# Performance work log

Measured on AMD Instinct MI355X. Metric: run time of the kernel, lower is better.

The kernel has to match this reference:

```python
import jax, jax.numpy as jnp
import numpy as np

B = 262144
INPUT_SIZE = 128
HIDDEN_SIZE = 128
EPS = 1e-08


def rms_norm(x, eps=EPS):
    # NB: despite the name, the original subtracts the mean (LayerNorm without affine)
    mean = jnp.mean(x, axis=-1, keepdims=True)
    var = jnp.var(x, axis=-1, keepdims=True)  # biased, matches unbiased=False
    return (x - mean) / jnp.sqrt(var + eps)


def activation_quant(x):
    s = 127.0 / jnp.max(jnp.abs(x), axis=-1, keepdims=True)
    return jnp.clip(jnp.round(s * x), -128.0, 127.0) / s


def matmul_free_linear(x, w_t):
    # w_t is ternary {-1,0,1}, shape [in, out]; original uses two masked matmuls
    pos = (w_t == 1.0).astype(x.dtype)
    neg = (w_t == -1.0).astype(x.dtype)
    return x @ pos - x @ neg


def setup_inputs() -> dict:
    key = jax.random.key(0)
    k1, k2, k3, k4, k5 = jax.random.split(key, 5)
    return {
        "x_t": jax.random.normal(k1, (B, INPUT_SIZE), dtype=jnp.float32),
        "h_t_minus_1": jax.random.normal(k2, (B, HIDDEN_SIZE), dtype=jnp.float32),
        "W_f": jax.random.normal(k3, (HIDDEN_SIZE, INPUT_SIZE), dtype=jnp.float32) * 0.01,
        "W_c": jax.random.normal(k4, (HIDDEN_SIZE, INPUT_SIZE), dtype=jnp.float32) * 0.01,
        "W_g": jax.random.normal(k5, (HIDDEN_SIZE, INPUT_SIZE), dtype=jnp.float32) * 0.01,
        "b_f": jnp.zeros((HIDDEN_SIZE,), dtype=jnp.float32),
        "b_c": jnp.zeros((HIDDEN_SIZE,), dtype=jnp.float32),
        "b_g": jnp.zeros((HIDDEN_SIZE,), dtype=jnp.float32),
    }


def reference(x_t, h_t_minus_1, W_f, W_c, W_g, b_f, b_c, b_g):
    x = activation_quant(rms_norm(x_t, EPS))
    Wf_t = jnp.sign(W_f).T  # [in, hidden]
    Wc_t = jnp.sign(W_c).T
    Wg_t = jnp.sign(W_g).T
    f_t = jax.nn.sigmoid(matmul_free_linear(x, Wf_t) + b_f)
    c_t = jax.nn.silu(matmul_free_linear(x, Wc_t) + b_c)
    g_t = jax.nn.sigmoid(matmul_free_linear(x, Wg_t) + b_g)
    h_t = f_t * h_t_minus_1 + (1.0 - f_t) * c_t
    o_t = g_t * h_t
    return (o_t, h_t)
```

## Files before the change

### kernel.cpp

```cpp
#include <hip/hip_runtime.h>
#include <math.h>

#define WPB 4
#define RG  8

__device__ __forceinline__ int dot4(int a, int b, int c) {
#if defined(__has_builtin)
#if __has_builtin(__builtin_amdgcn_sdot4)
    return __builtin_amdgcn_sdot4(a, b, c, false);
#define DOT4_DONE 1
#endif
#endif
#ifndef DOT4_DONE
    int r = c;
    r += ((a << 24) >> 24) * ((b << 24) >> 24);
    r += ((a << 16) >> 24) * ((b << 16) >> 24);
    r += ((a <<  8) >> 24) * ((b <<  8) >> 24);
    r += ( a        >> 24) * ( b        >> 24);
    return r;
#endif
}

__device__ __forceinline__ float sigmoidf_(float v) {
    return 1.0f / (1.0f + __expf(-v));
}

__global__ __launch_bounds__(256, 3)
void mlgru_kernel(const float* __restrict__ x,
                  const float* __restrict__ hprev,
                  const float* __restrict__ Wf,
                  const float* __restrict__ Wc,
                  const float* __restrict__ Wg,
                  const float* __restrict__ bf,
                  const float* __restrict__ bc,
                  const float* __restrict__ bg,
                  float* __restrict__ out,
                  int nrows)
{
    __shared__ int   wlds[3 * 32 * 128];
    __shared__ short qlds[WPB][RG][64];

    const int tid  = threadIdx.x;
    const int lane = tid & 63;
    const int widx = tid >> 6;

    for (int idx = tid; idx < 3 * 4096; idx += 256) {
        const int g   = idx >> 12;
        const int rem = idx & 4095;
        const int j   = rem >> 5;
        const int w   = rem & 31;
        const float* Wp = (g == 0) ? Wf : ((g == 1) ? Wc : Wg);
        const float4 v = *(const float4*)(Wp + j * 128 + w * 4);
        const int b0 = (v.x > 0.f) - (v.x < 0.f);
        const int b1 = (v.y > 0.f) - (v.y < 0.f);
        const int b2 = (v.z > 0.f) - (v.z < 0.f);
        const int b3 = (v.w > 0.f) - (v.w < 0.f);
        wlds[g * 4096 + w * 128 + j] =
            (b0 & 0xFF) | ((b1 & 0xFF) << 8) | ((b2 & 0xFF) << 16) | ((b3 & 0xFF) << 24);
    }

    const float2 vbf = *(const float2*)(bf + 2 * lane);
    const float2 vbc = *(const float2*)(bc + 2 * lane);
    const float2 vbg = *(const float2*)(bg + 2 * lane);
    __syncthreads();

    const int gw   = blockIdx.x * WPB + widx;
    const int nw   = gridDim.x * WPB;
    const int ngrp = nrows / RG;
    const long long hoff = (long long)nrows * 128;

    for (int grp = gw; grp < ngrp; grp += nw) {
        const int row0 = grp * RG;

        float invs[RG];
        float2 xv[RG];
        #pragma unroll
        for (int r = 0; r < RG; ++r)
            xv[r] = *(const float2*)(x + (long long)(row0 + r) * 128 + 2 * lane);

        #pragma unroll
        for (int r = 0; r < RG; ++r) {
            float s  = xv[r].x + xv[r].y;
            float ss = xv[r].x * xv[r].x + xv[r].y * xv[r].y;
            #pragma unroll
            for (int off = 32; off >= 1; off >>= 1) {
                s  += __shfl_xor(s, off);
                ss += __shfl_xor(ss, off);
            }
            const float mean = s * (1.0f / 128.0f);
            const float var  = ss * (1.0f / 128.0f) - mean * mean;
            const float rstd = rsqrtf(var + 1e-8f);
            const float y0 = (xv[r].x - mean) * rstd;
            const float y1 = (xv[r].y - mean) * rstd;
            float a = fmaxf(fabsf(y0), fabsf(y1));
            #pragma unroll
            for (int off = 32; off >= 1; off >>= 1)
                a = fmaxf(a, __shfl_xor(a, off));
            const float sq = 127.0f / a;
            invs[r] = a * (1.0f / 127.0f);
            int q0 = (int)rintf(y0 * sq);
            int q1 = (int)rintf(y1 * sq);
            q0 = max(-128, min(127, q0));
            q1 = max(-128, min(127, q1));
            qlds[widx][r][lane] = (short)((q0 & 0xFF) | ((q1 & 0xFF) << 8));
        }
        __asm__ __volatile__("s_waitcnt lgkmcnt(0)" ::: "memory");

        int acc[3][2][RG];
        #pragma unroll
        for (int g = 0; g < 3; ++g)
            #pragma unroll
            for (int h = 0; h < 2; ++h)
                #pragma unroll
                for (int r = 0; r < RG; ++r)
                    acc[g][h][r] = 0;

        const int* qrow = (const int*)(&qlds[widx][0][0]);

        #pragma unroll 2
        for (int w4 = 0; w4 < 8; ++w4) {
            int qa[RG][4];
            #pragma unroll
            for (int r = 0; r < RG; ++r) {
                const int4 t = *(const int4*)(qrow + r * 32 + w4 * 4);
                qa[r][0] = t.x; qa[r][1] = t.y; qa[r][2] = t.z; qa[r][3] = t.w;
            }
            #pragma unroll
            for (int wi = 0; wi < 4; ++wi) {
                const int w = w4 * 4 + wi;
                #pragma unroll
                for (int g = 0; g < 3; ++g) {
                    const int2 wv = *(const int2*)(&wlds[g * 4096 + w * 128 + 2 * lane]);
                    #pragma unroll
                    for (int r = 0; r < RG; ++r) {
                        acc[g][0][r] = dot4(qa[r][wi], wv.x, acc[g][0][r]);
                        acc[g][1][r] = dot4(qa[r][wi], wv.y, acc[g][1][r]);
                    }
                }
            }
        }

        #pragma unroll
        for (int r = 0; r < RG; ++r) {
            const long long rbase = (long long)(row0 + r) * 128 + 2 * lane;
            const float2 hp = *(const float2*)(hprev + rbase);
            const float inv = invs[r];

            const float f0 = sigmoidf_((float)acc[0][0][r] * inv + vbf.x);
            const float f1 = sigmoidf_((float)acc[0][1][r] * inv + vbf.y);
            const float cx0 = (float)acc[1][0][r] * inv + vbc.x;
            const float cx1 = (float)acc[1][1][r] * inv + vbc.y;
            const float c0 = cx0 * sigmoidf_(cx0);
            const float c1 = cx1 * sigmoidf_(cx1);
            const float g0 = sigmoidf_((float)acc[2][0][r] * inv + vbg.x);
            const float g1 = sigmoidf_((float)acc[2][1][r] * inv + vbg.y);

            const float h0 = f0 * hp.x + (1.0f - f0) * c0;
            const float h1 = f1 * hp.y + (1.0f - f1) * c1;
            const float o0 = g0 * h0;
            const float o1 = g1 * h1;

            *(float2*)(out + rbase)        = make_float2(o0, o1);
            *(float2*)(out + hoff + rbase) = make_float2(h0, h1);
        }
    }
}

extern "C" void kernel_launch(void* const* d_in, const int* in_sizes, int n_in,
                              void* d_out, int out_size, void* d_ws, size_t ws_size,
                              hipStream_t stream) {
    const float* x  = (const float*)d_in[0];
    const float* h  = (const float*)d_in[1];
    const float* Wf = (const float*)d_in[2];
    const float* Wc = (const float*)d_in[3];
    const float* Wg = (const float*)d_in[4];
    const float* bf = (const float*)d_in[5];
    const float* bc = (const float*)d_in[6];
    const float* bg = (const float*)d_in[7];
    float* out = (float*)d_out;
    const int nrows = in_sizes[0] / 128;

    hipLaunchKernelGGL(mlgru_kernel, dim3(768), dim3(256), 0, stream,
                       x, h, Wf, Wc, Wg, bf, bc, bg, out, nrows);
}
```

Before: 543.3 us.

## Replace sdot4 int8 GEMM with MFMA i32_16x16x64_i8 matrix cores

```diff
diff --git a/kernel.cpp b/kernel.cpp
--- a/kernel.cpp
+++ b/kernel.cpp
@@ -1,25 +1,8 @@
 #include <hip/hip_runtime.h>
 #include <math.h>
 
-#define WPB 4
-#define RG  8
-
-__device__ __forceinline__ int dot4(int a, int b, int c) {
-#if defined(__has_builtin)
-#if __has_builtin(__builtin_amdgcn_sdot4)
-    return __builtin_amdgcn_sdot4(a, b, c, false);
-#define DOT4_DONE 1
-#endif
-#endif
-#ifndef DOT4_DONE
-    int r = c;
-    r += ((a << 24) >> 24) * ((b << 24) >> 24);
-    r += ((a << 16) >> 24) * ((b << 16) >> 24);
-    r += ((a <<  8) >> 24) * ((b <<  8) >> 24);
-    r += ( a        >> 24) * ( b        >> 24);
-    return r;
-#endif
-}
+typedef __attribute__((ext_vector_type(4))) int   i32x4;
+typedef __attribute__((ext_vector_type(4))) float f32x4;
 
 __device__ __forceinline__ float sigmoidf_(float v) {
     return 1.0f / (1.0f + __expf(-v));
@@ -37,131 +20,145 @@
                   float* __restrict__ out,
                   int nrows)
 {
-    __shared__ int   wlds[3 * 32 * 128];
-    __shared__ short qlds[WPB][RG][64];
+    __shared__ i32x4 wlds[3 * 8 * 2 * 64];
 
     const int tid  = threadIdx.x;
     const int lane = tid & 63;
     const int widx = tid >> 6;
+    const int lm   = lane & 15;
+    const int kg   = lane >> 4;
 
-    for (int idx = tid; idx < 3 * 4096; idx += 256) {
-        const int g   = idx >> 12;
-        const int rem = idx & 4095;
-        const int j   = rem >> 5;
-        const int w   = rem & 31;
+    for (int idx = tid; idx < 3 * 8 * 2 * 64; idx += 256) {
+        const int l  = idx & 63;
+        const int s  = (idx >> 6) & 1;
+        const int t  = (idx >> 7) & 7;
+        const int g  = idx >> 10;
         const float* Wp = (g == 0) ? Wf : ((g == 1) ? Wc : Wg);
-        const float4 v = *(const float4*)(Wp + j * 128 + w * 4);
-        const int b0 = (v.x > 0.f) - (v.x < 0.f);
-        const int b1 = (v.y > 0.f) - (v.y < 0.f);
-        const int b2 = (v.z > 0.f) - (v.z < 0.f);
-        const int b3 = (v.w > 0.f) - (v.w < 0.f);
-        wlds[g * 4096 + w * 128 + j] =
-            (b0 & 0xFF) | ((b1 & 0xFF) << 8) | ((b2 & 0xFF) << 16) | ((b3 & 0xFF) << 24);
+        const int n  = t * 16 + (l & 15);
+        const int kb = s * 64 + (l >> 4) * 16;
+        i32x4 fr;
+        #pragma unroll
+        for (int d = 0; d < 4; ++d) {
+            const float4 v = *(const float4*)(Wp + n * 128 + kb + d * 4);
+            const int b0 = (v.x > 0.f) - (v.x < 0.f);
+            const int b1 = (v.y > 0.f) - (v.y < 0.f);
+            const int b2 = (v.z > 0.f) - (v.z < 0.f);
+            const int b3 = (v.w > 0.f) - (v.w < 0.f);
+            fr[d] = (b0 & 0xFF) | ((b1 & 0xFF) << 8) | ((b2 & 0xFF) << 16) | ((b3 & 0xFF) << 24);
+        }
+        wlds[idx] = fr;
     }
 
-    const float2 vbf = *(const float2*)(bf + 2 * lane);
-    const float2 vbc = *(const float2*)(bc + 2 * lane);
-    const float2 vbg = *(const float2*)(bg + 2 * lane);
+    float vbf[8], vbc[8], vbg[8];
+    #pragma unroll
+    for (int t = 0; t < 8; ++t) {
+        vbf[t] = bf[t * 16 + lm];
+        vbc[t] = bc[t * 16 + lm];
+        vbg[t] = bg[t * 16 + lm];
+    }
     __syncthreads();
 
-    const int gw   = blockIdx.x * WPB + widx;
-    const int nw   = gridDim.x * WPB;
-    const int ngrp = nrows / RG;
+    const int gw   = blockIdx.x * 4 + widx;
+    const int nw   = gridDim.x * 4;
+    const int ngrp = nrows >> 5;
     const long long hoff = (long long)nrows * 128;
 
     for (int grp = gw; grp < ngrp; grp += nw) {
-        const int row0 = grp * RG;
+        const int row0 = grp << 5;
 
-        float invs[RG];
-        float2 xv[RG];
-        #pragma unroll
-        for (int r = 0; r < RG; ++r)
-            xv[r] = *(const float2*)(x + (long long)(row0 + r) * 128 + 2 * lane);
+        i32x4 afrag[2][2];
+        float invm[2];
 
         #pragma unroll
-        for (int r = 0; r < RG; ++r) {
-            float s  = xv[r].x + xv[r].y;
-            float ss = xv[r].x * xv[r].x + xv[r].y * xv[r].y;
+        for (int mt = 0; mt < 2; ++mt) {
+            const float* xr = x + (long long)(row0 + mt * 16 + lm) * 128 + kg * 16;
+            f32x4 vv[8];
             #pragma unroll
-            for (int off = 32; off >= 1; off >>= 1) {
-                s  += __shfl_xor(s, off);
-                ss += __shfl_xor(ss, off);
+            for (int j = 0; j < 4; ++j) {
+                vv[j]     = *(const f32x4*)(xr + j * 4);
+                vv[j + 4] = *(const f32x4*)(xr + 64 + j * 4);
             }
+            float s = 0.f, ss = 0.f;
+            #pragma unroll
+            for (int j = 0; j < 8; ++j)
+                #pragma unroll
+                for (int e = 0; e < 4; ++e) { const float t = vv[j][e]; s += t; ss = fmaf(t, t, ss); }
+            s  += __shfl_xor(s, 16);   ss += __shfl_xor(ss, 16);
+            s  += __shfl_xor(s, 32);   ss += __shfl_xor(ss, 32);
             const float mean = s * (1.0f / 128.0f);
             const float var  = ss * (1.0f / 128.0f) - mean * mean;
             const float rstd = rsqrtf(var + 1e-8f);
-            const float y0 = (xv[r].x - mean) * rstd;
-            const float y1 = (xv[r].y - mean) * rstd;
-            float a = fmaxf(fabsf(y0), fabsf(y1));
+            float am = 0.f;
             #pragma unroll
-            for (int off = 32; off >= 1; off >>= 1)
-                a = fmaxf(a, __shfl_xor(a, off));
-            const float sq = 127.0f / a;
-            invs[r] = a * (1.0f / 127.0f);
-            int q0 = (int)rintf(y0 * sq);
-            int q1 = (int)rintf(y1 * sq);
-            q0 = max(-128, min(127, q0));
-            q1 = max(-128, min(127, q1));
-            qlds[widx][r][lane] = (short)((q0 & 0xFF) | ((q1 & 0xFF) << 8));
-        }
-        __asm__ __volatile__("s_waitcnt lgkmcnt(0)" ::: "memory");
-
-        int acc[3][2][RG];
-        #pragma unroll
-        for (int g = 0; g < 3; ++g)
+            for (int j = 0; j < 8; ++j)
+                #pragma unroll
+                for (int e = 0; e < 4; ++e) {
+                    const float t = vv[j][e] - mean;
+                    vv[j][e] = t;
+                    am = fmaxf(am, fabsf(t));
+                }
+            am = fmaxf(am, __shfl_xor(am, 16));
+            am = fmaxf(am, __shfl_xor(am, 32));
+            const float sq = 127.0f / am;
+            invm[mt] = am * rstd * (1.0f / 127.0f);
             #pragma unroll
-            for (int h = 0; h < 2; ++h)
+            for (int s2 = 0; s2 < 2; ++s2) {
+                i32x4 fr;
                 #pragma unroll
-                for (int r = 0; r < RG; ++r)
-                    acc[g][h][r] = 0;
-
-        const int* qrow = (const int*)(&qlds[widx][0][0]);
-
-        #pragma unroll 2
-        for (int w4 = 0; w4 < 8; ++w4) {
-            int qa[RG][4];
-            #pragma unroll
-            for (int r = 0; r < RG; ++r) {
-                const int4 t = *(const int4*)(qrow + r * 32 + w4 * 4);
-                qa[r][0] = t.x; qa[r][1] = t.y; qa[r][2] = t.z; qa[r][3] = t.w;
-            }
-            #pragma unroll
-            for (int wi = 0; wi < 4; ++wi) {
-                const int w = w4 * 4 + wi;
-                #pragma unroll
-                for (int g = 0; g < 3; ++g) {
-                    const int2 wv = *(const int2*)(&wlds[g * 4096 + w * 128 + 2 * lane]);
-                    #pragma unroll
-                    for (int r = 0; r < RG; ++r) {
-                        acc[g][0][r] = dot4(qa[r][wi], wv.x, acc[g][0][r]);
-                        acc[g][1][r] = dot4(qa[r][wi], wv.y, acc[g][1][r]);
-                    }
+                for (int d = 0; d < 4; ++d) {
+                    const int j = s2 * 4 + d;
+                    const int q0 = max(-128, min(127, (int)rintf(vv[j][0] * sq)));
+                    const int q1 = max(-128, min(127, (int)rintf(vv[j][1] * sq)));
+                    const int q2 = max(-128, min(127, (int)rintf(vv[j][2] * sq)));
+                    const int q3 = max(-128, min(127, (int)rintf(vv[j][3] * sq)));
+                    fr[d] = (q0 & 0xFF) | ((q1 & 0xFF) << 8) | ((q2 & 0xFF) << 16) | ((q3 & 0xFF) << 24);
                 }
+                afrag[mt][s2] = fr;
             }
         }
 
+        float invb[2][4];
         #pragma unroll
-        for (int r = 0; r < RG; ++r) {
-            const long long rbase = (long long)(row0 + r) * 128 + 2 * lane;
-            const float2 hp = *(const float2*)(hprev + rbase);
-            const float inv = invs[r];
+        for (int mt = 0; mt < 2; ++mt)
+            #pragma unroll
+            for (int r = 0; r < 4; ++r)
+                invb[mt][r] = __shfl(invm[mt], kg * 4 + r);
 
-            const float f0 = sigmoidf_((float)acc[0][0][r] * inv + vbf.x);
-            const float f1 = sigmoidf_((float)acc[0][1][r] * inv + vbf.y);
-            const float cx0 = (float)acc[1][0][r] * inv + vbc.x;
-            const float cx1 = (float)acc[1][1][r] * inv + vbc.y;
-            const float c0 = cx0 * sigmoidf_(cx0);
-            const float c1 = cx1 * sigmoidf_(cx1);
-            const float g0 = sigmoidf_((float)acc[2][0][r] * inv + vbg.x);
-            const float g1 = sigmoidf_((float)acc[2][1][r] * inv + vbg.y);
+        for (int t = 0; t < 8; ++t) {
+            i32x4 acc[3][2];
+            #pragma unroll
+            for (int g = 0; g < 3; ++g) {
+                acc[g][0] = (i32x4){0, 0, 0, 0};
+                acc[g][1] = (i32x4){0, 0, 0, 0};
+            }
+            #pragma unroll
+            for (int s2 = 0; s2 < 2; ++s2)
+                #pragma unroll
+                for (int g = 0; g < 3; ++g) {
+                    const i32x4 bfr = wlds[((g * 8 + t) * 2 + s2) * 64 + lane];
+                    acc[g][0] = __builtin_amdgcn_mfma_i32_16x16x64_i8(afrag[0][s2], bfr, acc[g][0], 0, 0, 0);
+                    acc[g][1] = __builtin_amdgcn_mfma_i32_16x16x64_i8(afrag[1][s2], bfr, acc[g][1], 0, 0, 0);
+                }
 
-            const float h0 = f0 * hp.x + (1.0f - f0) * c0;
-            const float h1 = f1 * hp.y + (1.0f - f1) * c1;
-            const float o0 = g0 * h0;
-            const float o1 = g1 * h1;
-
-            *(float2*)(out + rbase)        = make_float2(o0, o1);
-            *(float2*)(out + hoff + rbase) = make_float2(h0, h1);
+            #pragma unroll
+            for (int mt = 0; mt < 2; ++mt)
+                #pragma unroll
+                for (int r = 0; r < 4; ++r) {
+                    const int m = kg * 4 + r;
+                    const float inv = invb[mt][r];
+                    const long long rbase =
+                        (long long)(row0 + mt * 16 + m) * 128 + t * 16 + lm;
+                    const float hp = hprev[rbase];
+                    const float fx = (float)acc[0][mt][r] * inv + vbf[t];
+                    const float cx = (float)acc[1][mt][r] * inv + vbc[t];
+                    const float gx = (float)acc[2][mt][r] * inv + vbg[t];
+                    const float f  = sigmoidf_(fx);
+                    const float c  = cx * sigmoidf_(cx);
+                    const float gg = sigmoidf_(gx);
+                    const float h  = f * hp + (1.0f - f) * c;
+                    out[rbase]        = gg * h;
+                    out[hoff + rbase] = h;
+                }
         }
     }
 }
@@ -180,6 +177,6 @@
     float* out = (float*)d_out;
     const int nrows = in_sizes[0] / 128;
 
-    hipLaunchKernelGGL(mlgru_kernel, dim3(768), dim3(256), 0, stream,
+    hipLaunchKernelGGL(mlgru_kernel, dim3(1024), dim3(256), 0, stream,
                        x, h, Wf, Wc, Wg, bf, bc, bg, out, nrows);
 }
```

After: 515.0 us. 1.05x faster.
